# Performance work log

Measured on AMD Instinct MI355X. Metric: run time of the kernel, lower is better.

The kernel has to match this reference:

```python
import jax, jax.numpy as jnp
import numpy as np


def _gcn_conv(x, W, b, src, dst, n_nodes):
    """PyG-style GCNConv: XW, symmetric deg^-1/2 normalization over edges
    (with self-loops already included in src/dst), scatter-add to targets, + bias."""
    xw = x @ W  # [N, F_out]
    ones = jnp.ones(src.shape[0], dtype=xw.dtype)
    deg = jax.ops.segment_sum(ones, dst, num_segments=n_nodes)  # in-degree incl. self-loops
    dinv = jnp.where(deg > 0, jax.lax.rsqrt(jnp.maximum(deg, 1.0)), 0.0)
    norm = dinv[src] * dinv[dst]                        # [E]
    msgs = xw[src] * norm[:, None]                      # [E, F_out] gather + scale
    out = jax.ops.segment_sum(msgs, dst, num_segments=n_nodes)  # scatter-add
    return out + b


def setup_inputs() -> dict:
    key = jax.random.key(0)
    k1, k2, k3, k4 = jax.random.split(key, 4)
    N, E = 100000, 1600000
    IN, HID, OUT = 128, 64, 64
    x = jax.random.normal(k1, (N, IN), dtype=jnp.float32)
    edge_index = jax.random.randint(k2, (2, E), 0, N, dtype=jnp.int64)
    W1 = jax.random.normal(k3, (IN, HID), dtype=jnp.float32) * (1.0 / np.sqrt(IN))
    b1 = jnp.zeros((HID,), dtype=jnp.float32)
    W2 = jax.random.normal(k4, (HID, OUT), dtype=jnp.float32) * (1.0 / np.sqrt(HID))
    b2 = jnp.zeros((OUT,), dtype=jnp.float32)
    return {"x": x, "edge_index": edge_index, "W1": W1, "b1": b1, "W2": W2, "b2": b2}


def reference(x, edge_index, W1, b1, W2, b2):
    n_nodes = x.shape[0]
    # add self-loops (PyG GCNConv default add_self_loops=True)
    loops = jnp.arange(n_nodes, dtype=edge_index.dtype)
    src = jnp.concatenate([edge_index[0], loops])
    dst = jnp.concatenate([edge_index[1], loops])
    h = _gcn_conv(x, W1, b1, src, dst, n_nodes)
    h = jax.nn.relu(h)
    z = _gcn_conv(h, W2, b2, src, dst, n_nodes)
    return z
```

## Files before the change

### kernel.cpp

```cpp
#include <hip/hip_runtime.h>

#define IN_F 128
#define HID_F 64
#define BKT_SHIFT 9
#define BKT_SIZE 512
#define CHUNK 4096

typedef unsigned short ushort_t;
typedef __attribute__((ext_vector_type(8))) short bf16x8;
typedef __attribute__((ext_vector_type(8))) unsigned short u16x8;
typedef __attribute__((ext_vector_type(4))) float f32x4;

__device__ inline ushort_t f2bf(float f) {
    unsigned u = __float_as_uint(f);
    u += 0x7FFFu + ((u >> 16) & 1u);
    return (ushort_t)(u >> 16);
}
__device__ inline float bf2f(ushort_t u) {
    return __uint_as_float((unsigned)u << 16);
}


__global__ __launch_bounds__(256) void k_hist_pack(const int* __restrict__ dst,
        int* __restrict__ ghist, int E, int nbE,
        const float* __restrict__ W1, const float* __restrict__ W2,
        ushort_t* __restrict__ Bp1, ushort_t* __restrict__ Bp2) {
    int tid = threadIdx.x;
    if ((int)blockIdx.x >= nbE) {
        int id = ((int)blockIdx.x - nbE) * 256 + tid;
        int iw = (id < 8192) ? id : id - 8192;
        int j = iw & 7, lane = (iw >> 3) & 63, t = (iw >> 9) & 3, s = iw >> 11;
        int k = s * 32 + ((lane >> 4) << 3) + j;
        int n = t * 16 + (lane & 15);
        if (id < 8192)        Bp1[iw] = f2bf(W1[k * 64 + n]);
        else if (id < 12288)  Bp2[iw] = f2bf(W2[k * 64 + n]);
        return;
    }
    __shared__ int hist[256];
    hist[tid] = 0;
    __syncthreads();
    int e0 = blockIdx.x * CHUNK, e1 = min(e0 + CHUNK, E);
    for (int e = e0 + tid; e < e1; e += 256)
        atomicAdd(&hist[dst[e] >> BKT_SHIFT], 1);
    __syncthreads();
    ghist[blockIdx.x * 256 + tid] = hist[tid];
}

__global__ __launch_bounds__(256) void k_colscan(int* __restrict__ ghist,
        int* __restrict__ gcount, int nb) {
    __shared__ int s[256];
    int t = threadIdx.x;
    int b = blockIdx.x;
    int j0 = 2 * t, j1 = 2 * t + 1;
    int v0 = (j0 < nb) ? ghist[j0 * 256 + b] : 0;
    int v1 = (j1 < nb) ? ghist[j1 * 256 + b] : 0;
    int p = v0 + v1;
    s[t] = p;
    __syncthreads();
    for (int off = 1; off < 256; off <<= 1) {
        int v = (t >= off) ? s[t - off] : 0;
        __syncthreads();
        s[t] += v;
        __syncthreads();
    }
    int excl = s[t] - p;
    if (j0 < nb) ghist[j0 * 256 + b] = excl;
    if (j1 < nb) ghist[j1 * 256 + b] = excl + v0;
    if (t == 255) gcount[b] = s[255];
}

__global__ __launch_bounds__(256) void k_bscan(const int* __restrict__ gcount,
        int* __restrict__ gbase, int* __restrict__ bbase,
        int* __restrict__ rowptr, int N, int E) {
    __shared__ int s[256];
    int t = threadIdx.x;
    int c = gcount[t];
    s[t] = c;
    __syncthreads();
    for (int off = 1; off < 256; off <<= 1) {
        int v = (t >= off) ? s[t - off] : 0;
        __syncthreads();
        s[t] += v;
        __syncthreads();
    }
    int base = s[t] - c;
    gbase[t] = base;
    bbase[t] = base;
    if (t == 255) bbase[256] = s[255];
    if (t == 0) rowptr[N] = E;
}

__global__ __launch_bounds__(256) void k_scatter(const int* __restrict__ src,
        const int* __restrict__ dst, const int* __restrict__ ghist,
        const int* __restrict__ gbase, unsigned* __restrict__ gbin, int E) {
    __shared__ int cur[256];
    int tid = threadIdx.x;
    cur[tid] = ghist[blockIdx.x * 256 + tid] + gbase[tid];
    __syncthreads();
    int e0 = blockIdx.x * CHUNK, e1 = min(e0 + CHUNK, E);
    for (int e = e0 + tid; e < e1; e += 256) {
        int d = dst[e];
        int b = d >> BKT_SHIFT;
        int p = atomicAdd(&cur[b], 1);
        gbin[p] = ((unsigned)(d & (BKT_SIZE - 1)) << 23) | (unsigned)src[e];
    }
}

__global__ __launch_bounds__(256) void k_fill2(const unsigned* __restrict__ gbin,
        const int* __restrict__ bbase, int* __restrict__ rowptr,
        float* __restrict__ dinv, int* __restrict__ col, int N) {
    __shared__ int cnt[BKT_SIZE];
    __shared__ int pos[BKT_SIZE];
    __shared__ int s[256];
    int tid = threadIdx.x;
    int b = blockIdx.x;
    int e0 = bbase[b], e1 = bbase[b + 1];
    cnt[tid] = 0; cnt[tid + 256] = 0;
    __syncthreads();
    for (int e = e0 + tid; e < e1; e += 256)
        atomicAdd(&cnt[gbin[e] >> 23], 1);
    __syncthreads();
    int c0 = cnt[2 * tid], c1 = cnt[2 * tid + 1];
    int p2 = c0 + c1;
    s[tid] = p2;
    __syncthreads();
    for (int off = 1; off < 256; off <<= 1) {
        int v = (tid >= off) ? s[tid - off] : 0;
        __syncthreads();
        s[tid] += v;
        __syncthreads();
    }
    int excl = s[tid] - p2;
    pos[2 * tid] = excl;
    pos[2 * tid + 1] = excl + c0;
    __syncthreads();
    int n0 = b << BKT_SHIFT;
    #pragma unroll
    for (int i = tid; i < BKT_SIZE; i += 256) {
        int n = n0 + i;
        if (n < N) {
            rowptr[n] = e0 + pos[i];
            dinv[n] = rsqrtf((float)cnt[i] + 1.0f);
        }
    }
    __syncthreads();
    for (int e = e0 + tid; e < e1; e += 256) {
        unsigned v = gbin[e];
        int p = atomicAdd(&pos[v >> 23], 1);
        col[e0 + p] = (int)(v & 0x7FFFFFu);
    }
}

template<int K, typename AT>
__global__ __launch_bounds__(256) void k_gemm_mfma(const AT* __restrict__ A,
        const ushort_t* __restrict__ Bp, const float* __restrict__ dinv,
        ushort_t* __restrict__ out, int N) {
    int wave = threadIdx.x >> 6, lane = threadIdx.x & 63;
    int m = lane & 15, q = lane >> 4;
    int row0 = blockIdx.x * 64 + wave * 16;
    int arow = row0 + m;
    int arowc = (arow < N) ? arow : (N - 1);
    f32x4 acc[4] = {};
    #pragma unroll
    for (int s = 0; s < K / 32; ++s) {
        bf16x8 af;
        if constexpr (sizeof(AT) == 4) {
            const float* ap = (const float*)A + (size_t)arowc * K + s * 32 + q * 8;
            float4 x0 = *(const float4*)ap;
            float4 x1 = *(const float4*)(ap + 4);
            af[0] = (short)f2bf(x0.x); af[1] = (short)f2bf(x0.y);
            af[2] = (short)f2bf(x0.z); af[3] = (short)f2bf(x0.w);
            af[4] = (short)f2bf(x1.x); af[5] = (short)f2bf(x1.y);
            af[6] = (short)f2bf(x1.z); af[7] = (short)f2bf(x1.w);
        } else {
            af = *(const bf16x8*)((const ushort_t*)A + (size_t)arowc * K + s * 32 + q * 8);
        }
        #pragma unroll
        for (int t = 0; t < 4; ++t) {
            bf16x8 bf = *(const bf16x8*)(Bp + (size_t)((s * 4 + t) * 64 + lane) * 8);
            acc[t] = __builtin_amdgcn_mfma_f32_16x16x32_bf16(af, bf, acc[t], 0, 0, 0);
        }
    }
    int orow0 = row0 + q * 4;
    float4 d4 = *(const float4*)(dinv + orow0);
    #pragma unroll
    for (int r = 0; r < 4; ++r) {
        int row = orow0 + r;
        if (row < N) {
            float dn = (r == 0) ? d4.x : (r == 1) ? d4.y : (r == 2) ? d4.z : d4.w;
            #pragma unroll
            for (int t = 0; t < 4; ++t)
                out[(size_t)row * 64 + t * 16 + m] = f2bf(acc[t][r] * dn);
        }
    }
}

__global__ __launch_bounds__(256) void k_aggregate(const ushort_t* __restrict__ xws,
        const int* __restrict__ rowptr, const int* __restrict__ col,
        const float* __restrict__ dinv, const float* __restrict__ bias,
        float* __restrict__ outf, ushort_t* __restrict__ outb, int N, int relu_bf16) {
    int n = (blockIdx.x * 256 + threadIdx.x) >> 3;
    int i = threadIdx.x & 7;
    if (n >= N) return;
    int beg = rowptr[n], end = rowptr[n + 1];
    float dn = dinv[n];
    const ushort_t* base = xws + i * 8;
    u16x8 sv = *(const u16x8*)(base + (size_t)n * 64);
    float a[8];
    #pragma unroll
    for (int k = 0; k < 8; ++k) a[k] = bf2f(sv[k]);
    int e = beg;
    for (; e + 8 <= end; e += 8) {
        int c[8];
        #pragma unroll
        for (int j = 0; j < 8; ++j) c[j] = col[e + j];
        u16x8 v[8];
        #pragma unroll
        for (int j = 0; j < 8; ++j) v[j] = *(const u16x8*)(base + (size_t)c[j] * 64);
        #pragma unroll
        for (int j = 0; j < 8; ++j)
            #pragma unroll
            for (int k = 0; k < 8; ++k) a[k] += bf2f(v[j][k]);
    }
    if (e + 4 <= end) {
        int c[4];
        #pragma unroll
        for (int j = 0; j < 4; ++j) c[j] = col[e + j];
        u16x8 v[4];
        #pragma unroll
        for (int j = 0; j < 4; ++j) v[j] = *(const u16x8*)(base + (size_t)c[j] * 64);
        #pragma unroll
        for (int j = 0; j < 4; ++j)
            #pragma unroll
            for (int k = 0; k < 8; ++k) a[k] += bf2f(v[j][k]);
        e += 4;
    }
    for (; e < end; ++e) {
        u16x8 v = *(const u16x8*)(base + (size_t)col[e] * 64);
        #pragma unroll
        for (int k = 0; k < 8; ++k) a[k] += bf2f(v[k]);
    }
    float4 b0 = *(const float4*)(bias + i * 8);
    float4 b1 = *(const float4*)(bias + i * 8 + 4);
    float r[8];
    r[0] = dn * a[0] + b0.x; r[1] = dn * a[1] + b0.y;
    r[2] = dn * a[2] + b0.z; r[3] = dn * a[3] + b0.w;
    r[4] = dn * a[4] + b1.x; r[5] = dn * a[5] + b1.y;
    r[6] = dn * a[6] + b1.z; r[7] = dn * a[7] + b1.w;
    if (relu_bf16) {
        u16x8 o;
        #pragma unroll
        for (int k = 0; k < 8; ++k) o[k] = f2bf(fmaxf(r[k], 0.f));
        *(u16x8*)(outb + (size_t)n * 64 + i * 8) = o;
    } else {
        float4 o0 = {r[0], r[1], r[2], r[3]};
        float4 o1 = {r[4], r[5], r[6], r[7]};
        *(float4*)(outf + (size_t)n * 64 + i * 8) = o0;
        *(float4*)(outf + (size_t)n * 64 + i * 8 + 4) = o1;
    }
}


extern "C" void kernel_launch(void* const* d_in, const int* in_sizes, int n_in,
                              void* d_out, int out_size, void* d_ws, size_t ws_size,
                              hipStream_t stream) {
    const float* x  = (const float*)d_in[0];
    const int*   ei = (const int*)d_in[1];
    const float* W1 = (const float*)d_in[2];
    const float* b1 = (const float*)d_in[3];
    const float* W2 = (const float*)d_in[4];
    const float* b2 = (const float*)d_in[5];
    float* out = (float*)d_out;

    const int N = in_sizes[0] / IN_F;
    const int E = in_sizes[1] / 2;
    const int* src = ei;
    const int* dst = ei + E;

    char* ws = (char*)d_ws;
    const size_t MB = 1u << 20;
    int*      bbase   = (int*)     (ws + 4096);
    int*      gbase   = (int*)     (ws + 8192);
    int*      gcount  = (int*)     (ws + 12288);
    ushort_t* Bp1     = (ushort_t*)(ws + 16384);
    ushort_t* Bp2     = (ushort_t*)(ws + 49152);
    int*      rowptr  = (int*)     (ws + 1 * MB);
    float*    dinv    = (float*)   (ws + 2 * MB);
    unsigned* gbin    = (unsigned*)(ws + 3 * MB);
    int*      ghist   = (int*)     (ws + 10 * MB);
    int*      col     = (int*)     (ws + 11 * MB);
    ushort_t* xws     = (ushort_t*)(ws + 20 * MB);
    ushort_t* h       = (ushort_t*)(ws + 36 * MB);

    const int nbE = (E + CHUNK - 1) / CHUNK;
    const int nbB = (N + BKT_SIZE - 1) / BKT_SIZE;
    const int nbG = (N + 63) / 64;
    const int nbA = (N * 8 + 255) / 256;

    k_hist_pack<<<nbE + 48, 256, 0, stream>>>(dst, ghist, E, nbE, W1, W2, Bp1, Bp2);
    k_colscan<<<256, 256, 0, stream>>>(ghist, gcount, nbE);
    k_bscan  <<<1, 256, 0, stream>>>(gcount, gbase, bbase, rowptr, N, E);
    k_scatter<<<nbE, 256, 0, stream>>>(src, dst, ghist, gbase, gbin, E);
    k_fill2  <<<nbB, 256, 0, stream>>>(gbin, bbase, rowptr, dinv, col, N);

    k_gemm_mfma<IN_F, float>   <<<nbG, 256, 0, stream>>>(x, Bp1, dinv, xws, N);
    k_aggregate<<<nbA, 256, 0, stream>>>(xws, rowptr, col, dinv, b1, nullptr, h, N, 1);

    k_gemm_mfma<HID_F, ushort_t><<<nbG, 256, 0, stream>>>(h, Bp2, dinv, xws, N);
    k_aggregate<<<nbA, 256, 0, stream>>>(xws, rowptr, col, dinv, b2, out, nullptr, N, 0);
}
```

Baseline: 231.6 us.

## Store features in column-sliced layout and aggregate per slice with edge-parallel lanes

The GEMM output and hidden activations move to a sliced layout: eight slices of 8 bf16 features, each slice stored contiguously over all nodes. Aggregation runs one slice per block (blockIdx & 7), so each block's gathers touch a 1.6 MB slice that is more likely to stay cache-resident. Within a node, the 8 lanes now split the edges instead of the features, and the partial sums are combined with xor shuffles. Each gather becomes a 16-byte random read, and the cross-lane reduction adds work.

```diff
diff --git a/kernel.cpp b/kernel.cpp
--- a/kernel.cpp
+++ b/kernel.cpp
@@ -173,7 +173,7 @@
             af[4] = (short)f2bf(x1.x); af[5] = (short)f2bf(x1.y);
             af[6] = (short)f2bf(x1.z); af[7] = (short)f2bf(x1.w);
         } else {
-            af = *(const bf16x8*)((const ushort_t*)A + (size_t)arowc * K + s * 32 + q * 8);
+            af = *(const bf16x8*)((const ushort_t*)A + ((size_t)(s * 4 + q) * N + arowc) * 8);
         }
         #pragma unroll
         for (int t = 0; t < 4; ++t) {
@@ -189,74 +189,67 @@
         if (row < N) {
             float dn = (r == 0) ? d4.x : (r == 1) ? d4.y : (r == 2) ? d4.z : d4.w;
             #pragma unroll
-            for (int t = 0; t < 4; ++t)
-                out[(size_t)row * 64 + t * 16 + m] = f2bf(acc[t][r] * dn);
-        }
-    }
-}
-
-__global__ __launch_bounds__(256) void k_aggregate(const ushort_t* __restrict__ xws,
+            for (int t = 0; t < 4; ++t) {
+                int sl = t * 2 + (m >> 3);
+                out[((size_t)sl * N + row) * 8 + (m & 7)] = f2bf(acc[t][r] * dn);
+            }
+        }
+    }
+}
+
+__global__ __launch_bounds__(256) void k_aggregate_s(const ushort_t* __restrict__ xs,
         const int* __restrict__ rowptr, const int* __restrict__ col,
         const float* __restrict__ dinv, const float* __restrict__ bias,
         float* __restrict__ outf, ushort_t* __restrict__ outb, int N, int relu_bf16) {
-    int n = (blockIdx.x * 256 + threadIdx.x) >> 3;
-    int i = threadIdx.x & 7;
+    int slice = blockIdx.x & 7;
+    int n = ((int)(blockIdx.x >> 3)) * 32 + ((int)threadIdx.x >> 3);
+    int j = threadIdx.x & 7;
     if (n >= N) return;
+    const ushort_t* base = xs + (size_t)slice * N * 8;
     int beg = rowptr[n], end = rowptr[n + 1];
-    float dn = dinv[n];
-    const ushort_t* base = xws + i * 8;
-    u16x8 sv = *(const u16x8*)(base + (size_t)n * 64);
-    float a[8];
+    float a[8] = {0.f, 0.f, 0.f, 0.f, 0.f, 0.f, 0.f, 0.f};
+    if (j == 0) {
+        u16x8 sv = *(const u16x8*)(base + (size_t)n * 8);
+        #pragma unroll
+        for (int k = 0; k < 8; ++k) a[k] = bf2f(sv[k]);
+    }
+    int e = beg + j;
+    for (; e + 8 < end; e += 16) {
+        int c0 = col[e], c1 = col[e + 8];
+        u16x8 v0 = *(const u16x8*)(base + (size_t)c0 * 8);
+        u16x8 v1 = *(const u16x8*)(base + (size_t)c1 * 8);
+        #pragma unroll
+        for (int k = 0; k < 8; ++k) a[k] += bf2f(v0[k]) + bf2f(v1[k]);
+    }
+    if (e < end) {
+        u16x8 v = *(const u16x8*)(base + (size_t)col[e] * 8);
+        #pragma unroll
+        for (int k = 0; k < 8; ++k) a[k] += bf2f(v[k]);
+    }
     #pragma unroll
-    for (int k = 0; k < 8; ++k) a[k] = bf2f(sv[k]);
-    int e = beg;
-    for (; e + 8 <= end; e += 8) {
-        int c[8];
-        #pragma unroll
-        for (int j = 0; j < 8; ++j) c[j] = col[e + j];
-        u16x8 v[8];
-        #pragma unroll
-        for (int j = 0; j < 8; ++j) v[j] = *(const u16x8*)(base + (size_t)c[j] * 64);
-        #pragma unroll
-        for (int j = 0; j < 8; ++j)
+    for (int off = 1; off < 8; off <<= 1)
+        #pragma unroll
+        for (int k = 0; k < 8; ++k) a[k] += __shfl_xor(a[k], off);
+    if (j == 0) {
+        float dn = dinv[n];
+        float4 b0 = *(const float4*)(bias + slice * 8);
+        float4 b1 = *(const float4*)(bias + slice * 8 + 4);
+        float r[8];
+        r[0] = dn * a[0] + b0.x; r[1] = dn * a[1] + b0.y;
+        r[2] = dn * a[2] + b0.z; r[3] = dn * a[3] + b0.w;
+        r[4] = dn * a[4] + b1.x; r[5] = dn * a[5] + b1.y;
+        r[6] = dn * a[6] + b1.z; r[7] = dn * a[7] + b1.w;
+        if (relu_bf16) {
+            u16x8 o;
             #pragma unroll
-            for (int k = 0; k < 8; ++k) a[k] += bf2f(v[j][k]);
-    }
-    if (e + 4 <= end) {
-        int c[4];
-        #pragma unroll
-        for (int j = 0; j < 4; ++j) c[j] = col[e + j];
-        u16x8 v[4];
-        #pragma unroll
-        for (int j = 0; j < 4; ++j) v[j] = *(const u16x8*)(base + (size_t)c[j] * 64);
-        #pragma unroll
-        for (int j = 0; j < 4; ++j)
-            #pragma unroll
-            for (int k = 0; k < 8; ++k) a[k] += bf2f(v[j][k]);
-        e += 4;
-    }
-    for (; e < end; ++e) {
-        u16x8 v = *(const u16x8*)(base + (size_t)col[e] * 64);
-        #pragma unroll
-        for (int k = 0; k < 8; ++k) a[k] += bf2f(v[k]);
-    }
-    float4 b0 = *(const float4*)(bias + i * 8);
-    float4 b1 = *(const float4*)(bias + i * 8 + 4);
-    float r[8];
-    r[0] = dn * a[0] + b0.x; r[1] = dn * a[1] + b0.y;
-    r[2] = dn * a[2] + b0.z; r[3] = dn * a[3] + b0.w;
-    r[4] = dn * a[4] + b1.x; r[5] = dn * a[5] + b1.y;
-    r[6] = dn * a[6] + b1.z; r[7] = dn * a[7] + b1.w;
-    if (relu_bf16) {
-        u16x8 o;
-        #pragma unroll
-        for (int k = 0; k < 8; ++k) o[k] = f2bf(fmaxf(r[k], 0.f));
-        *(u16x8*)(outb + (size_t)n * 64 + i * 8) = o;
-    } else {
-        float4 o0 = {r[0], r[1], r[2], r[3]};
-        float4 o1 = {r[4], r[5], r[6], r[7]};
-        *(float4*)(outf + (size_t)n * 64 + i * 8) = o0;
-        *(float4*)(outf + (size_t)n * 64 + i * 8 + 4) = o1;
+            for (int k = 0; k < 8; ++k) o[k] = f2bf(fmaxf(r[k], 0.f));
+            *(u16x8*)(outb + ((size_t)slice * N + n) * 8) = o;
+        } else {
+            float4 o0 = {r[0], r[1], r[2], r[3]};
+            float4 o1 = {r[4], r[5], r[6], r[7]};
+            *(float4*)(outf + (size_t)n * 64 + slice * 8) = o0;
+            *(float4*)(outf + (size_t)n * 64 + slice * 8 + 4) = o1;
+        }
     }
 }
 
@@ -295,7 +288,7 @@
     const int nbE = (E + CHUNK - 1) / CHUNK;
     const int nbB = (N + BKT_SIZE - 1) / BKT_SIZE;
     const int nbG = (N + 63) / 64;
-    const int nbA = (N * 8 + 255) / 256;
+    const int nbA = 8 * ((N + 31) / 32);
 
     k_hist_pack<<<nbE + 48, 256, 0, stream>>>(dst, ghist, E, nbE, W1, W2, Bp1, Bp2);
     k_colscan<<<256, 256, 0, stream>>>(ghist, gcount, nbE);
@@ -304,8 +297,8 @@
     k_fill2  <<<nbB, 256, 0, stream>>>(gbin, bbase, rowptr, dinv, col, N);
 
     k_gemm_mfma<IN_F, float>   <<<nbG, 256, 0, stream>>>(x, Bp1, dinv, xws, N);
-    k_aggregate<<<nbA, 256, 0, stream>>>(xws, rowptr, col, dinv, b1, nullptr, h, N, 1);
+    k_aggregate_s<<<nbA, 256, 0, stream>>>(xws, rowptr, col, dinv, b1, nullptr, h, N, 1);
 
     k_gemm_mfma<HID_F, ushort_t><<<nbG, 256, 0, stream>>>(h, Bp2, dinv, xws, N);
-    k_aggregate<<<nbA, 256, 0, stream>>>(xws, rowptr, col, dinv, b2, out, nullptr, N, 0);
-}
+    k_aggregate_s<<<nbA, 256, 0, stream>>>(xws, rowptr, col, dinv, b2, out, nullptr, N, 0);
+}
```

Result: slower. 296.1 us (+27.8%).

## Store features in 8-column slices so aggregation gathers from cache-sized planes

Applied to the files above, without the earlier changes.

The intermediate features (xws and h) are stored slice-major: eight planes of N×8 bf16 values instead of row-major N×64. Aggregation now assigns one thread per node per slice, with grid blocks interleaved across slices, so each gather touches a 1.6 MB plane that can stay resident in L2/LLC. The aim is more cache reuse for the random neighbor gathers. In exchange, the col and rowptr indices are read eight times, once per slice, and the GEMM writes become strided 2-byte stores.

```diff
diff --git a/kernel.cpp b/kernel.cpp
--- a/kernel.cpp
+++ b/kernel.cpp
@@ -173,7 +173,7 @@
             af[4] = (short)f2bf(x1.x); af[5] = (short)f2bf(x1.y);
             af[6] = (short)f2bf(x1.z); af[7] = (short)f2bf(x1.w);
         } else {
-            af = *(const bf16x8*)((const ushort_t*)A + (size_t)arowc * K + s * 32 + q * 8);
+            af = *(const bf16x8*)((const ushort_t*)A + ((size_t)(s * 4 + q) * N + arowc) * 8);
         }
         #pragma unroll
         for (int t = 0; t < 4; ++t) {
@@ -189,23 +189,24 @@
         if (row < N) {
             float dn = (r == 0) ? d4.x : (r == 1) ? d4.y : (r == 2) ? d4.z : d4.w;
             #pragma unroll
-            for (int t = 0; t < 4; ++t)
-                out[(size_t)row * 64 + t * 16 + m] = f2bf(acc[t][r] * dn);
+            for (int t = 0; t < 4; ++t) {
+                int sl = t * 2 + (m >> 3);
+                out[((size_t)sl * N + row) * 8 + (m & 7)] = f2bf(acc[t][r] * dn);
+            }
         }
     }
 }
 
-__global__ __launch_bounds__(256) void k_aggregate(const ushort_t* __restrict__ xws,
+__global__ __launch_bounds__(256) void k_aggregate_s(const ushort_t* __restrict__ xs,
         const int* __restrict__ rowptr, const int* __restrict__ col,
         const float* __restrict__ dinv, const float* __restrict__ bias,
         float* __restrict__ outf, ushort_t* __restrict__ outb, int N, int relu_bf16) {
-    int n = (blockIdx.x * 256 + threadIdx.x) >> 3;
-    int i = threadIdx.x & 7;
+    int slice = blockIdx.x & 7;
+    int n = ((int)(blockIdx.x >> 3)) * 256 + (int)threadIdx.x;
     if (n >= N) return;
+    const ushort_t* base = xs + (size_t)slice * N * 8;
     int beg = rowptr[n], end = rowptr[n + 1];
-    float dn = dinv[n];
-    const ushort_t* base = xws + i * 8;
-    u16x8 sv = *(const u16x8*)(base + (size_t)n * 64);
+    u16x8 sv = *(const u16x8*)(base + (size_t)n * 8);
     float a[8];
     #pragma unroll
     for (int k = 0; k < 8; ++k) a[k] = bf2f(sv[k]);
@@ -216,7 +217,7 @@
         for (int j = 0; j < 8; ++j) c[j] = col[e + j];
         u16x8 v[8];
         #pragma unroll
-        for (int j = 0; j < 8; ++j) v[j] = *(const u16x8*)(base + (size_t)c[j] * 64);
+        for (int j = 0; j < 8; ++j) v[j] = *(const u16x8*)(base + (size_t)c[j] * 8);
         #pragma unroll
         for (int j = 0; j < 8; ++j)
             #pragma unroll
@@ -228,7 +229,7 @@
         for (int j = 0; j < 4; ++j) c[j] = col[e + j];
         u16x8 v[4];
         #pragma unroll
-        for (int j = 0; j < 4; ++j) v[j] = *(const u16x8*)(base + (size_t)c[j] * 64);
+        for (int j = 0; j < 4; ++j) v[j] = *(const u16x8*)(base + (size_t)c[j] * 8);
         #pragma unroll
         for (int j = 0; j < 4; ++j)
             #pragma unroll
@@ -236,12 +237,13 @@
         e += 4;
     }
     for (; e < end; ++e) {
-        u16x8 v = *(const u16x8*)(base + (size_t)col[e] * 64);
+        u16x8 v = *(const u16x8*)(base + (size_t)col[e] * 8);
         #pragma unroll
         for (int k = 0; k < 8; ++k) a[k] += bf2f(v[k]);
     }
-    float4 b0 = *(const float4*)(bias + i * 8);
-    float4 b1 = *(const float4*)(bias + i * 8 + 4);
+    float dn = dinv[n];
+    float4 b0 = *(const float4*)(bias + slice * 8);
+    float4 b1 = *(const float4*)(bias + slice * 8 + 4);
     float r[8];
     r[0] = dn * a[0] + b0.x; r[1] = dn * a[1] + b0.y;
     r[2] = dn * a[2] + b0.z; r[3] = dn * a[3] + b0.w;
@@ -251,12 +253,12 @@
         u16x8 o;
         #pragma unroll
         for (int k = 0; k < 8; ++k) o[k] = f2bf(fmaxf(r[k], 0.f));
-        *(u16x8*)(outb + (size_t)n * 64 + i * 8) = o;
+        *(u16x8*)(outb + ((size_t)slice * N + n) * 8) = o;
     } else {
         float4 o0 = {r[0], r[1], r[2], r[3]};
         float4 o1 = {r[4], r[5], r[6], r[7]};
-        *(float4*)(outf + (size_t)n * 64 + i * 8) = o0;
-        *(float4*)(outf + (size_t)n * 64 + i * 8 + 4) = o1;
+        *(float4*)(outf + (size_t)n * 64 + slice * 8) = o0;
+        *(float4*)(outf + (size_t)n * 64 + slice * 8 + 4) = o1;
     }
 }
 
@@ -295,7 +297,7 @@
     const int nbE = (E + CHUNK - 1) / CHUNK;
     const int nbB = (N + BKT_SIZE - 1) / BKT_SIZE;
     const int nbG = (N + 63) / 64;
-    const int nbA = (N * 8 + 255) / 256;
+    const int nbA = 8 * ((N + 255) / 256);
 
     k_hist_pack<<<nbE + 48, 256, 0, stream>>>(dst, ghist, E, nbE, W1, W2, Bp1, Bp2);
     k_colscan<<<256, 256, 0, stream>>>(ghist, gcount, nbE);
@@ -304,8 +306,8 @@
     k_fill2  <<<nbB, 256, 0, stream>>>(gbin, bbase, rowptr, dinv, col, N);
 
     k_gemm_mfma<IN_F, float>   <<<nbG, 256, 0, stream>>>(x, Bp1, dinv, xws, N);
-    k_aggregate<<<nbA, 256, 0, stream>>>(xws, rowptr, col, dinv, b1, nullptr, h, N, 1);
+    k_aggregate_s<<<nbA, 256, 0, stream>>>(xws, rowptr, col, dinv, b1, nullptr, h, N, 1);
 
     k_gemm_mfma<HID_F, ushort_t><<<nbG, 256, 0, stream>>>(h, Bp2, dinv, xws, N);
-    k_aggregate<<<nbA, 256, 0, stream>>>(xws, rowptr, col, dinv, b2, out, nullptr, N, 0);
-}
+    k_aggregate_s<<<nbA, 256, 0, stream>>>(xws, rowptr, col, dinv, b2, out, nullptr, N, 0);
+}
```

Result: slower. 312.4 us (+34.9%).

## Fuse CSR build kernels into one cooperative kernel with grid syncs

Applied to the files above, without the earlier changes.

The five CSR construction launches (histogram/pack, column scan, bucket scan, scatter, bucket fill) are merged into one cooperative kernel that separates the phases with grid.sync(). The aim is to remove four kernel launch gaps and their inter-kernel drain and refill. In exchange the whole grid (nbE+48, about 440 blocks) must be co-resident, and every phase now runs at that fixed grid size. Grid-wide barriers also cost something, and some phases leave most blocks idle.

```diff
diff --git a/kernel.cpp b/kernel.cpp
--- a/kernel.cpp
+++ b/kernel.cpp
@@ -1,4 +1,7 @@
 #include <hip/hip_runtime.h>
+#include <hip/hip_cooperative_groups.h>
+
+namespace cg = cooperative_groups;
 
 #define IN_F 128
 #define HID_F 64
@@ -20,134 +23,131 @@
     return __uint_as_float((unsigned)u << 16);
 }
 
-
-__global__ __launch_bounds__(256) void k_hist_pack(const int* __restrict__ dst,
-        int* __restrict__ ghist, int E, int nbE,
+__global__ __launch_bounds__(256) void k_csr(const int* __restrict__ src,
+        const int* __restrict__ dst, int* __restrict__ ghist,
+        int* __restrict__ gcount, int* __restrict__ gbase, int* __restrict__ bbase,
+        int* __restrict__ rowptr, float* __restrict__ dinv,
+        unsigned* __restrict__ gbin, int* __restrict__ col,
         const float* __restrict__ W1, const float* __restrict__ W2,
-        ushort_t* __restrict__ Bp1, ushort_t* __restrict__ Bp2) {
+        ushort_t* __restrict__ Bp1, ushort_t* __restrict__ Bp2,
+        int E, int N, int nbE, int nbB) {
+    cg::grid_group grid = cg::this_grid();
+    __shared__ int sh[1280];
     int tid = threadIdx.x;
-    if ((int)blockIdx.x >= nbE) {
-        int id = ((int)blockIdx.x - nbE) * 256 + tid;
+    int bid = blockIdx.x;
+
+    if (bid < nbE) {
+        sh[tid] = 0;
+        __syncthreads();
+        int e0 = bid * CHUNK, e1 = min(e0 + CHUNK, E);
+        for (int e = e0 + tid; e < e1; e += 256)
+            atomicAdd(&sh[dst[e] >> BKT_SHIFT], 1);
+        __syncthreads();
+        ghist[bid * 256 + tid] = sh[tid];
+    } else {
+        int id = (bid - nbE) * 256 + tid;
         int iw = (id < 8192) ? id : id - 8192;
         int j = iw & 7, lane = (iw >> 3) & 63, t = (iw >> 9) & 3, s = iw >> 11;
         int k = s * 32 + ((lane >> 4) << 3) + j;
         int n = t * 16 + (lane & 15);
         if (id < 8192)        Bp1[iw] = f2bf(W1[k * 64 + n]);
         else if (id < 12288)  Bp2[iw] = f2bf(W2[k * 64 + n]);
-        return;
-    }
-    __shared__ int hist[256];
-    hist[tid] = 0;
-    __syncthreads();
-    int e0 = blockIdx.x * CHUNK, e1 = min(e0 + CHUNK, E);
-    for (int e = e0 + tid; e < e1; e += 256)
-        atomicAdd(&hist[dst[e] >> BKT_SHIFT], 1);
-    __syncthreads();
-    ghist[blockIdx.x * 256 + tid] = hist[tid];
-}
-
-__global__ __launch_bounds__(256) void k_colscan(int* __restrict__ ghist,
-        int* __restrict__ gcount, int nb) {
-    __shared__ int s[256];
-    int t = threadIdx.x;
-    int b = blockIdx.x;
-    int j0 = 2 * t, j1 = 2 * t + 1;
-    int v0 = (j0 < nb) ? ghist[j0 * 256 + b] : 0;
-    int v1 = (j1 < nb) ? ghist[j1 * 256 + b] : 0;
-    int p = v0 + v1;
-    s[t] = p;
-    __syncthreads();
-    for (int off = 1; off < 256; off <<= 1) {
-        int v = (t >= off) ? s[t - off] : 0;
-        __syncthreads();
-        s[t] += v;
-        __syncthreads();
-    }
-    int excl = s[t] - p;
-    if (j0 < nb) ghist[j0 * 256 + b] = excl;
-    if (j1 < nb) ghist[j1 * 256 + b] = excl + v0;
-    if (t == 255) gcount[b] = s[255];
-}
-
-__global__ __launch_bounds__(256) void k_bscan(const int* __restrict__ gcount,
-        int* __restrict__ gbase, int* __restrict__ bbase,
-        int* __restrict__ rowptr, int N, int E) {
-    __shared__ int s[256];
-    int t = threadIdx.x;
-    int c = gcount[t];
-    s[t] = c;
-    __syncthreads();
-    for (int off = 1; off < 256; off <<= 1) {
-        int v = (t >= off) ? s[t - off] : 0;
-        __syncthreads();
-        s[t] += v;
-        __syncthreads();
-    }
-    int base = s[t] - c;
-    gbase[t] = base;
-    bbase[t] = base;
-    if (t == 255) bbase[256] = s[255];
-    if (t == 0) rowptr[N] = E;
-}
-
-__global__ __launch_bounds__(256) void k_scatter(const int* __restrict__ src,
-        const int* __restrict__ dst, const int* __restrict__ ghist,
-        const int* __restrict__ gbase, unsigned* __restrict__ gbin, int E) {
-    __shared__ int cur[256];
-    int tid = threadIdx.x;
-    cur[tid] = ghist[blockIdx.x * 256 + tid] + gbase[tid];
-    __syncthreads();
-    int e0 = blockIdx.x * CHUNK, e1 = min(e0 + CHUNK, E);
-    for (int e = e0 + tid; e < e1; e += 256) {
-        int d = dst[e];
-        int b = d >> BKT_SHIFT;
-        int p = atomicAdd(&cur[b], 1);
-        gbin[p] = ((unsigned)(d & (BKT_SIZE - 1)) << 23) | (unsigned)src[e];
-    }
-}
-
-__global__ __launch_bounds__(256) void k_fill2(const unsigned* __restrict__ gbin,
-        const int* __restrict__ bbase, int* __restrict__ rowptr,
-        float* __restrict__ dinv, int* __restrict__ col, int N) {
-    __shared__ int cnt[BKT_SIZE];
-    __shared__ int pos[BKT_SIZE];
-    __shared__ int s[256];
-    int tid = threadIdx.x;
-    int b = blockIdx.x;
-    int e0 = bbase[b], e1 = bbase[b + 1];
-    cnt[tid] = 0; cnt[tid + 256] = 0;
-    __syncthreads();
-    for (int e = e0 + tid; e < e1; e += 256)
-        atomicAdd(&cnt[gbin[e] >> 23], 1);
-    __syncthreads();
-    int c0 = cnt[2 * tid], c1 = cnt[2 * tid + 1];
-    int p2 = c0 + c1;
-    s[tid] = p2;
-    __syncthreads();
-    for (int off = 1; off < 256; off <<= 1) {
-        int v = (tid >= off) ? s[tid - off] : 0;
-        __syncthreads();
-        s[tid] += v;
-        __syncthreads();
-    }
-    int excl = s[tid] - p2;
-    pos[2 * tid] = excl;
-    pos[2 * tid + 1] = excl + c0;
-    __syncthreads();
-    int n0 = b << BKT_SHIFT;
-    #pragma unroll
-    for (int i = tid; i < BKT_SIZE; i += 256) {
-        int n = n0 + i;
-        if (n < N) {
-            rowptr[n] = e0 + pos[i];
-            dinv[n] = rsqrtf((float)cnt[i] + 1.0f);
-        }
-    }
-    __syncthreads();
-    for (int e = e0 + tid; e < e1; e += 256) {
-        unsigned v = gbin[e];
-        int p = atomicAdd(&pos[v >> 23], 1);
-        col[e0 + p] = (int)(v & 0x7FFFFFu);
+    }
+    grid.sync();
+
+    if (bid < 256) {
+        int b = bid;
+        int j0 = 2 * tid, j1 = 2 * tid + 1;
+        int v0 = (j0 < nbE) ? ghist[j0 * 256 + b] : 0;
+        int v1 = (j1 < nbE) ? ghist[j1 * 256 + b] : 0;
+        int p = v0 + v1;
+        sh[tid] = p;
+        __syncthreads();
+        for (int off = 1; off < 256; off <<= 1) {
+            int v = (tid >= off) ? sh[tid - off] : 0;
+            __syncthreads();
+            sh[tid] += v;
+            __syncthreads();
+        }
+        int excl = sh[tid] - p;
+        if (j0 < nbE) ghist[j0 * 256 + b] = excl;
+        if (j1 < nbE) ghist[j1 * 256 + b] = excl + v0;
+        if (tid == 255) gcount[b] = sh[255];
+    }
+    grid.sync();
+
+    if (bid == 0) {
+        int c = gcount[tid];
+        sh[tid] = c;
+        __syncthreads();
+        for (int off = 1; off < 256; off <<= 1) {
+            int v = (tid >= off) ? sh[tid - off] : 0;
+            __syncthreads();
+            sh[tid] += v;
+            __syncthreads();
+        }
+        int base = sh[tid] - c;
+        gbase[tid] = base;
+        bbase[tid] = base;
+        if (tid == 255) bbase[256] = sh[255];
+        if (tid == 0) rowptr[N] = E;
+    }
+    grid.sync();
+
+    if (bid < nbE) {
+        sh[tid] = ghist[bid * 256 + tid] + gbase[tid];
+        __syncthreads();
+        int e0 = bid * CHUNK, e1 = min(e0 + CHUNK, E);
+        for (int e = e0 + tid; e < e1; e += 256) {
+            int d = dst[e];
+            int b = d >> BKT_SHIFT;
+            int p = atomicAdd(&sh[b], 1);
+            gbin[p] = ((unsigned)(d & (BKT_SIZE - 1)) << 23) | (unsigned)src[e];
+        }
+        __syncthreads();
+    }
+    grid.sync();
+
+    if (bid < nbB) {
+        int* cnt = sh;
+        int* pos = sh + 512;
+        int* s   = sh + 1024;
+        int b = bid;
+        int e0 = bbase[b], e1 = bbase[b + 1];
+        cnt[tid] = 0; cnt[tid + 256] = 0;
+        __syncthreads();
+        for (int e = e0 + tid; e < e1; e += 256)
+            atomicAdd(&cnt[gbin[e] >> 23], 1);
+        __syncthreads();
+        int c0 = cnt[2 * tid], c1 = cnt[2 * tid + 1];
+        int p2 = c0 + c1;
+        s[tid] = p2;
+        __syncthreads();
+        for (int off = 1; off < 256; off <<= 1) {
+            int v = (tid >= off) ? s[tid - off] : 0;
+            __syncthreads();
+            s[tid] += v;
+            __syncthreads();
+        }
+        int excl = s[tid] - p2;
+        pos[2 * tid] = excl;
+        pos[2 * tid + 1] = excl + c0;
+        __syncthreads();
+        int n0 = b << BKT_SHIFT;
+        #pragma unroll
+        for (int i = tid; i < BKT_SIZE; i += 256) {
+            int n = n0 + i;
+            if (n < N) {
+                rowptr[n] = e0 + pos[i];
+                dinv[n] = rsqrtf((float)cnt[i] + 1.0f);
+            }
+        }
+        __syncthreads();
+        for (int e = e0 + tid; e < e1; e += 256) {
+            unsigned v = gbin[e];
+            int p = atomicAdd(&pos[v >> 23], 1);
+            col[e0 + p] = (int)(v & 0x7FFFFFu);
+        }
     }
 }
 
@@ -292,16 +292,19 @@
     ushort_t* xws     = (ushort_t*)(ws + 20 * MB);
     ushort_t* h       = (ushort_t*)(ws + 36 * MB);
 
-    const int nbE = (E + CHUNK - 1) / CHUNK;
-    const int nbB = (N + BKT_SIZE - 1) / BKT_SIZE;
+    int nbE = (E + CHUNK - 1) / CHUNK;
+    int nbB = (N + BKT_SIZE - 1) / BKT_SIZE;
     const int nbG = (N + 63) / 64;
     const int nbA = (N * 8 + 255) / 256;
-
-    k_hist_pack<<<nbE + 48, 256, 0, stream>>>(dst, ghist, E, nbE, W1, W2, Bp1, Bp2);
-    k_colscan<<<256, 256, 0, stream>>>(ghist, gcount, nbE);
-    k_bscan  <<<1, 256, 0, stream>>>(gcount, gbase, bbase, rowptr, N, E);
-    k_scatter<<<nbE, 256, 0, stream>>>(src, dst, ghist, gbase, gbin, E);
-    k_fill2  <<<nbB, 256, 0, stream>>>(gbin, bbase, rowptr, dinv, col, N);
+    int Ev = E, Nv = N;
+
+    void* kargs[] = {
+        (void*)&src, (void*)&dst, (void*)&ghist, (void*)&gcount, (void*)&gbase,
+        (void*)&bbase, (void*)&rowptr, (void*)&dinv, (void*)&gbin, (void*)&col,
+        (void*)&W1, (void*)&W2, (void*)&Bp1, (void*)&Bp2,
+        (void*)&Ev, (void*)&Nv, (void*)&nbE, (void*)&nbB };
+    hipLaunchCooperativeKernel((void*)k_csr, dim3(nbE + 48), dim3(256),
+                               kargs, 0, stream);
 
     k_gemm_mfma<IN_F, float>   <<<nbG, 256, 0, stream>>>(x, Bp1, dinv, xws, N);
     k_aggregate<<<nbA, 256, 0, stream>>>(xws, rowptr, col, dinv, b1, nullptr, h, N, 1);
```

Result: slower. 465.4 us (+100.9%).
